# Kernel optimization log

Measured on AMD Instinct MI355X. Metric: run time of the kernel, lower is better.

## Reference

```python
import jax, jax.numpy as jnp
import numpy as np

B, L, D = 2, 2048, 2048
H, HKV, HD = 32, 8, 64
EPS = 1e-5
THETA = 1000000.0


def rms_norm(x, w):
    # normalize over last dim (head_dim)
    return x * jax.lax.rsqrt(jnp.mean(x * x, axis=-1, keepdims=True) + EPS) * w


def apply_rope(t):
    # t: (B, heads, L, HD); non-traditional (half-split) RoPE, offset=0
    half = HD // 2
    inv_freq = THETA ** (-jnp.arange(0, HD, 2, dtype=jnp.float32) / HD)  # (half,)
    ang = jnp.arange(L, dtype=jnp.float32)[:, None] * inv_freq           # (L, half)
    cos, sin = jnp.cos(ang), jnp.sin(ang)
    x1, x2 = t[..., :half], t[..., half:]
    return jnp.concatenate([x1 * cos - x2 * sin, x2 * cos + x1 * sin], axis=-1)


def setup_inputs() -> dict:
    key = jax.random.key(0)
    ks = jax.random.split(key, 5)
    s = 0.02
    return {
        "x": jax.random.normal(ks[0], (B, L, D), dtype=jnp.float32),
        "Wq": jax.random.normal(ks[1], (D, H * HD), dtype=jnp.float32) * s,
        "Wk": jax.random.normal(ks[2], (D, HKV * HD), dtype=jnp.float32) * s,
        "Wv": jax.random.normal(ks[3], (D, HKV * HD), dtype=jnp.float32) * s,
        "Wo": jax.random.normal(ks[4], (H * HD, D), dtype=jnp.float32) * s,
        "q_norm_w": jnp.ones((HD,), dtype=jnp.float32),
        "k_norm_w": jnp.ones((HD,), dtype=jnp.float32),
    }


def reference(x, Wq, Wk, Wv, Wo, q_norm_w, k_norm_w):
    scale = HD ** -0.5
    g = H // HKV  # GQA group size
    # projections
    q = (x @ Wq).reshape(B, L, H, HD)
    k = (x @ Wk).reshape(B, L, HKV, HD)
    v = (x @ Wv).reshape(B, L, HKV, HD)
    # per-head RMSNorm, then to (B, heads, L, HD)
    q = jnp.transpose(rms_norm(q, q_norm_w), (0, 2, 1, 3))
    k = jnp.transpose(rms_norm(k, k_norm_w), (0, 2, 1, 3))
    v = jnp.transpose(v, (0, 2, 1, 3))
    # RoPE
    q = apply_rope(q)
    k = apply_rope(k)
    # grouped-query attention with causal mask
    qg = q.reshape(B, HKV, g, L, HD)
    scores = jnp.einsum('bhgqd,bhkd->bhgqk', qg, k) * scale  # (B,HKV,g,L,L)
    causal = jnp.tril(jnp.ones((L, L), dtype=bool))
    scores = jnp.where(causal, scores, jnp.finfo(scores.dtype).min)
    probs = jax.nn.softmax(scores, axis=-1)
    out = jnp.einsum('bhgqk,bhkd->bhgqd', probs, v)           # (B,HKV,g,L,HD)
    out = jnp.transpose(out.reshape(B, H, L, HD), (0, 2, 1, 3)).reshape(B, L, H * HD)
    return out @ Wo
```

## Files before the change

kernel.cpp:

```cpp
#include <hip/hip_runtime.h>
#include <math.h>
#include <stdint.h>

#define B_ 2
#define L_ 2048
#define D_ 2048
#define H_ 32
#define HKV_ 8
#define HD_ 64
#define EPS_ 1e-5f

typedef _Float16 half_t;
typedef __attribute__((ext_vector_type(8))) _Float16 half8_t;
typedef __attribute__((ext_vector_type(4))) _Float16 half4_t;
typedef __attribute__((ext_vector_type(4))) float float4_t;

typedef const __attribute__((address_space(1))) uint32_t glb_u32;
typedef __attribute__((address_space(3))) uint32_t lds_u32;
#define GLOAD_LDS16(gp, lp) \
  __builtin_amdgcn_global_load_lds((glb_u32*)(gp), (lds_u32*)(lp), 16, 0, 0)

__device__ __forceinline__ float4_t fmax4(float4_t a, float4_t b) {
  float4_t r;
  r[0] = fmaxf(a[0], b[0]); r[1] = fmaxf(a[1], b[1]);
  r[2] = fmaxf(a[2], b[2]); r[3] = fmaxf(a[3], b[3]);
  return r;
}

__global__ __launch_bounds__(256) void prep_all(
    const float* __restrict__ x,
    const float* __restrict__ Wq, const float* __restrict__ Wk,
    const float* __restrict__ Wv, const float* __restrict__ Wo,
    half_t* __restrict__ xh,
    half_t* __restrict__ Wqt, half_t* __restrict__ Wkt,
    half_t* __restrict__ Wvt, half_t* __restrict__ Wot)
{
  __shared__ float tile[64][65];
  const int t = threadIdx.x;
  int id = blockIdx.x;

  if (id < 4096) {
    size_t i = ((size_t)id * 256 + t) * 8;
    float4 v0 = *(const float4*)&x[i];
    float4 v1 = *(const float4*)&x[i + 4];
    half8_t h;
    h[0] = (half_t)v0.x; h[1] = (half_t)v0.y; h[2] = (half_t)v0.z; h[3] = (half_t)v0.w;
    h[4] = (half_t)v1.x; h[5] = (half_t)v1.y; h[6] = (half_t)v1.z; h[7] = (half_t)v1.w;
    *(half8_t*)&xh[i] = h;
    return;
  }
  id -= 4096;
  const float* W; half_t* Wt; int N;
  if (id < 1024)      { W = Wq; Wt = Wqt; N = 2048; }
  else if (id < 1280) { id -= 1024; W = Wk; Wt = Wkt; N = 512; }
  else if (id < 1536) { id -= 1280; W = Wv; Wt = Wvt; N = 512; }
  else                { id -= 1536; W = Wo; Wt = Wot; N = 2048; }
  const int K = 2048;
  int tk = id & 31, tn = id >> 5;
  int k0 = tk * 64, n0 = tn * 64;

  int rr = t >> 6, cc = t & 63;
#pragma unroll
  for (int i = 0; i < 16; i++)
    tile[rr + i * 4][cc] = W[(size_t)(k0 + rr + i * 4) * N + n0 + cc];
  __syncthreads();

  int rn = t >> 2, q4 = (t & 3) * 16;
  half8_t h0, h1;
#pragma unroll
  for (int u = 0; u < 8; u++) h0[u] = (half_t)tile[q4 + u][rn];
#pragma unroll
  for (int u = 0; u < 8; u++) h1[u] = (half_t)tile[q4 + 8 + u][rn];
  *(half8_t*)&Wt[(size_t)(n0 + rn) * K + k0 + q4]     = h0;
  *(half8_t*)&Wt[(size_t)(n0 + rn) * K + k0 + q4 + 8] = h1;
}

template <typename CT>
__device__ __forceinline__ void gemm_tile_f16(
    const half_t* __restrict__ A, const half_t* __restrict__ Bt,
    CT* __restrict__ C, int K, int ldc, int row0, int col0)
{
  __shared__ __align__(16) half_t As[128 * 32];
  __shared__ __align__(16) half_t Bs[128 * 32];
  const int t    = threadIdx.x;
  const int lane = t & 63;
  const int w    = t >> 6;
  const int quad = lane >> 4, c = lane & 15;
  const int wm = (w >> 1) * 64, wn = (w & 1) * 64;

  float4_t acc[4][4];
#pragma unroll
  for (int i = 0; i < 4; i++)
#pragma unroll
    for (int j = 0; j < 4; j++) acc[i][j] = (float4_t){0.f, 0.f, 0.f, 0.f};

  const int srow = w * 32 + (lane >> 2);
  const int scol = (lane & 3) * 8;
  const half_t* Ag0 = A  + (size_t)(row0 + srow) * K + scol;
  const half_t* Ag1 = Ag0 + (size_t)16 * K;
  const half_t* Bg0 = Bt + (size_t)(col0 + srow) * K + scol;
  const half_t* Bg1 = Bg0 + (size_t)16 * K;
  half_t* As_w0 = &As[(w * 32) * 32];
  half_t* As_w1 = &As[(w * 32 + 16) * 32];
  half_t* Bs_w0 = &Bs[(w * 32) * 32];
  half_t* Bs_w1 = &Bs[(w * 32 + 16) * 32];

  for (int k0 = 0; k0 < K; k0 += 32) {
    __syncthreads();
    GLOAD_LDS16(Ag0 + k0, As_w0);
    GLOAD_LDS16(Ag1 + k0, As_w1);
    GLOAD_LDS16(Bg0 + k0, Bs_w0);
    GLOAD_LDS16(Bg1 + k0, Bs_w1);
    __syncthreads();

    half8_t af[4], bf[4];
#pragma unroll
    for (int i = 0; i < 4; i++)
      af[i] = *(const half8_t*)&As[(wm + i * 16 + c) * 32 + quad * 8];
#pragma unroll
    for (int j = 0; j < 4; j++)
      bf[j] = *(const half8_t*)&Bs[(wn + j * 16 + c) * 32 + quad * 8];
#pragma unroll
    for (int i = 0; i < 4; i++)
#pragma unroll
      for (int j = 0; j < 4; j++)
        acc[i][j] = __builtin_amdgcn_mfma_f32_16x16x32_f16(af[i], bf[j], acc[i][j], 0, 0, 0);
  }

#pragma unroll
  for (int i = 0; i < 4; i++)
#pragma unroll
    for (int r = 0; r < 4; r++) {
      CT* Cp = C + (size_t)(row0 + wm + i * 16 + quad * 4 + r) * ldc + col0 + wn + c;
#pragma unroll
      for (int j = 0; j < 4; j++)
        Cp[j * 16] = (CT)acc[i][j][r];
    }
}

__global__ __launch_bounds__(256) void qkv_gemm_h(
    const half_t* __restrict__ xh,
    const half_t* __restrict__ Wqt, const half_t* __restrict__ Wkt,
    const half_t* __restrict__ Wvt,
    half_t* __restrict__ qh, half_t* __restrict__ kh, half_t* __restrict__ vh)
{
  int bx = blockIdx.x;
  const half_t* Bt; half_t* C; int ldc, col0;
  if (bx < 16)      { Bt = Wqt; C = qh; ldc = H_ * HD_;   col0 = bx * 128; }
  else if (bx < 20) { Bt = Wkt; C = kh; ldc = HKV_ * HD_; col0 = (bx - 16) * 128; }
  else              { Bt = Wvt; C = vh; ldc = HKV_ * HD_; col0 = (bx - 20) * 128; }
  gemm_tile_f16<half_t>(xh, Bt, C, D_, ldc, blockIdx.y * 128, col0);
}

__global__ __launch_bounds__(256) void out_gemm_h(
    const half_t* __restrict__ attn, const half_t* __restrict__ Wot,
    float* __restrict__ out)
{
  gemm_tile_f16<float>(attn, Wot, out, H_ * HD_, D_, blockIdx.y * 128, blockIdx.x * 128);
}

__device__ __forceinline__ void norm_rope_body(
    half_t* buf, const float* w, int wave, int nheads, int lognh,
    int lane, float oscale)
{
  int head  = wave & (nheads - 1);
  int token = wave >> lognh;
  int l     = token & (L_ - 1);

  size_t idx = (size_t)token * (nheads * HD_) + head * HD_ + lane;
  float x = (float)buf[idx];

  float ss = x * x;
#pragma unroll
  for (int off = 32; off; off >>= 1) ss += __shfl_xor(ss, off);
  float xn = x * rsqrtf(ss * (1.0f / HD_) + EPS_) * w[lane];

  float partner = __shfl_xor(xn, 32);
  int   fi = lane & 31;
  float inv_freq = exp2f((float)fi * -0.622862853f);
  float ang = (float)l * inv_freq;
  float cv = cosf(ang), sv = sinf(ang);
  float res = (lane < 32) ? (xn * cv - partner * sv) : (xn * cv + partner * sv);
  buf[idx] = (half_t)(res * oscale);
}

__global__ __launch_bounds__(256) void postproc(
    half_t* __restrict__ qh, half_t* __restrict__ kh,
    const half_t* __restrict__ vh, half_t* __restrict__ vt,
    const float* __restrict__ qw, const float* __restrict__ kw)
{
  const int t = threadIdx.x;
  int id = blockIdx.x;
  if (id < 32768) {
    int wave = id * 4 + (t >> 6);
    norm_rope_body(qh, qw, wave, H_, 5, t & 63, 0.180336880f);
    return;
  }
  id -= 32768;
  if (id < 8192) {
    int wave = id * 4 + (t >> 6);
    norm_rope_body(kh, kw, wave, HKV_, 3, t & 63, 1.0f);
    return;
  }
  id -= 8192;
  int kk0 = (id & 31) * 64, kvh = (id >> 5) & 7, b = id >> 8;
  int d = t >> 2, uu = t & 3;
  const half_t* src = vh + (size_t)(b * L_) * (HKV_ * HD_) + kvh * HD_ + d;
  half_t* dst = vt + ((size_t)((b * HKV_ + kvh) * HD_ + d)) * L_ + kk0 + uu * 16;
  half_t vals[16];
#pragma unroll
  for (int u = 0; u < 16; u++)
    vals[u] = src[(size_t)(kk0 + uu * 16 + u) * (HKV_ * HD_)];
#pragma unroll
  for (int u = 0; u < 16; u += 4)
    *(half4_t*)&dst[u] = *(half4_t*)&vals[u];
}

__global__ __launch_bounds__(512) void flash_mfma2(
    const half_t* __restrict__ Qh, const half_t* __restrict__ Kh,
    const half_t* __restrict__ Vt, half_t* __restrict__ Oa)
{
  __shared__ __align__(16) half_t Ks[64][72];
  __shared__ __align__(16) half_t Vs[64][72];
  __shared__ __align__(16) half_t Ps[128][72];
  __shared__ __align__(16) float  Ab[128];

  const int t    = threadIdx.x;
  const int w    = t >> 6;
  const int lane = t & 63;
  const int quad = lane >> 4;
  const int c    = lane & 15;
  const int h = blockIdx.y, b = blockIdx.z;
  const int kvh = h >> 2;

  const half_t* kbase = Kh + (size_t)(b * L_) * (HKV_ * HD_) + kvh * HD_;
  const half_t* vbase = Vt + (size_t)((b * HKV_ + kvh) * HD_) * L_;
  const int sr = t >> 3;
  const int su = (t & 7) * 8;

  for (int pass = 0; pass < 2; pass++) {
    const int qb  = pass ? (15 - (int)blockIdx.x) : (int)blockIdx.x;
    const int q0  = qb * 128;
    const int wq0 = q0 + w * 16;

    half8_t qf0, qf1;
    {
      const half_t* qp = Qh + ((size_t)(b * L_ + wq0 + c)) * (H_ * HD_) + h * HD_;
      qf0 = *(const half8_t*)&qp[quad * 8];
      qf1 = *(const half8_t*)&qp[32 + quad * 8];
    }

    float4_t o[4];
#pragma unroll
    for (int dt = 0; dt < 4; dt++) o[dt] = (float4_t){0.f, 0.f, 0.f, 0.f};
    float mm = -__builtin_inff();
    float ll = 0.f;

    half8_t kr, vr;
    kr = *(const half8_t*)(kbase + (size_t)sr * (HKV_ * HD_) + su);
    vr = *(const half8_t*)(vbase + (size_t)sr * L_ + su);

    const int last = (q0 + 127) >> 6;
    for (int kt = 0; kt <= last; kt++) {
      const int kk0 = kt * 64;
      __syncthreads();
      *(half8_t*)&Ks[sr][su] = kr;
      *(half8_t*)&Vs[sr][su] = vr;
      __syncthreads();
      if (kt < last) {
        kr = *(const half8_t*)(kbase + (size_t)(kk0 + 64 + sr) * (HKV_ * HD_) + su);
        vr = *(const half8_t*)(vbase + (size_t)sr * L_ + kk0 + 64 + su);
      }
      if (kk0 > wq0 + 15) continue;

      float4_t S[4];
#pragma unroll
      for (int tt = 0; tt < 4; tt++) {
        half8_t kf0 = *(const half8_t*)&Ks[tt * 16 + c][quad * 8];
        half8_t kf1 = *(const half8_t*)&Ks[tt * 16 + c][32 + quad * 8];
        float4_t s = (float4_t){0.f, 0.f, 0.f, 0.f};
        s = __builtin_amdgcn_mfma_f32_16x16x32_f16(kf0, qf0, s, 0, 0, 0);
        s = __builtin_amdgcn_mfma_f32_16x16x32_f16(kf1, qf1, s, 0, 0, 0);
        S[tt] = s;
      }

      if (kk0 + 63 > wq0) {
#pragma unroll
        for (int tt = 0; tt < 4; tt++) {
          int base = kk0 + tt * 16 + quad * 4 - (wq0 + c);
#pragma unroll
          for (int r = 0; r < 4; r++)
            if (base + r > 0) S[tt][r] = -__builtin_inff();
        }
      }

      {
        float4_t m4 = fmax4(fmax4(S[0], S[1]), fmax4(S[2], S[3]));
        float mloc = fmaxf(fmaxf(m4[0], m4[1]), fmaxf(m4[2], m4[3]));
        mloc = fmaxf(mloc, __shfl_xor(mloc, 16));
        mloc = fmaxf(mloc, __shfl_xor(mloc, 32));
        float mnew = fmaxf(mm, mloc);
        float al = exp2f(mm - mnew);
        mm = mnew;
#pragma unroll
        for (int tt = 0; tt < 4; tt++) {
#pragma unroll
          for (int r = 0; r < 4; r++) S[tt][r] = exp2f(S[tt][r] - mnew);
          half4_t pv;
#pragma unroll
          for (int r = 0; r < 4; r++) pv[r] = (half_t)S[tt][r];
          *(half4_t*)&Ps[w * 16 + c][tt * 16 + quad * 4] = pv;
        }
        float4_t s4 = S[0] + S[1] + S[2] + S[3];
        float ls = (s4[0] + s4[1]) + (s4[2] + s4[3]);
        ls += __shfl_xor(ls, 16);
        ls += __shfl_xor(ls, 32);
        ll = ll * al + ls;
        if (quad == 0) Ab[w * 16 + c] = al;
      }

      {
        float4_t av = *(const float4_t*)&Ab[w * 16 + quad * 4];
#pragma unroll
        for (int dt = 0; dt < 4; dt++)
#pragma unroll
          for (int r = 0; r < 4; r++) o[dt][r] *= av[r];
      }

      half8_t pf0 = *(const half8_t*)&Ps[w * 16 + c][quad * 8];
      half8_t pf1 = *(const half8_t*)&Ps[w * 16 + c][32 + quad * 8];
#pragma unroll
      for (int dt = 0; dt < 4; dt++) {
        half8_t vf0 = *(const half8_t*)&Vs[dt * 16 + c][quad * 8];
        half8_t vf1 = *(const half8_t*)&Vs[dt * 16 + c][32 + quad * 8];
        o[dt] = __builtin_amdgcn_mfma_f32_16x16x32_f16(pf0, vf0, o[dt], 0, 0, 0);
        o[dt] = __builtin_amdgcn_mfma_f32_16x16x32_f16(pf1, vf1, o[dt], 0, 0, 0);
      }
    }

    if (quad == 0) Ab[w * 16 + c] = ll;
    {
      float4_t lv = *(const float4_t*)&Ab[w * 16 + quad * 4];
#pragma unroll
      for (int r = 0; r < 4; r++) {
        float inv = 1.0f / lv[r];
        half_t* op = Oa + ((size_t)(b * L_ + wq0 + quad * 4 + r)) * (H_ * HD_)
                   + h * HD_ + c;
#pragma unroll
        for (int dt = 0; dt < 4; dt++)
          op[dt * 16] = (half_t)(o[dt][r] * inv);
      }
    }
  }
}

extern "C" void kernel_launch(void* const* d_in, const int* in_sizes, int n_in,
                              void* d_out, int out_size, void* d_ws, size_t ws_size,
                              hipStream_t stream)
{
  const float* x  = (const float*)d_in[0];
  const float* Wq = (const float*)d_in[1];
  const float* Wk = (const float*)d_in[2];
  const float* Wv = (const float*)d_in[3];
  const float* Wo = (const float*)d_in[4];
  const float* qw = (const float*)d_in[5];
  const float* kw = (const float*)d_in[6];
  float* out = (float*)d_out;

  const size_t XN = (size_t)B_ * L_ * D_;
  const size_t QN = (size_t)B_ * L_ * H_ * HD_;
  const size_t KN = (size_t)B_ * L_ * HKV_ * HD_;
  const size_t WQ = (size_t)D_ * H_ * HD_;
  const size_t WK = (size_t)D_ * HKV_ * HD_;

  half_t* p   = (half_t*)d_ws;
  half_t* xh  = p;  p += XN;
  half_t* Wqt = p;  p += WQ;
  half_t* Wkt = p;  p += WK;
  half_t* Wvt = p;  p += WK;
  half_t* Wot = p;  p += WQ;
  half_t* qh  = p;  p += QN;
  half_t* kh  = p;  p += KN;
  half_t* vh  = p;  p += KN;
  half_t* vt  = p;  p += KN;
  half_t* attn = xh;

  prep_all<<<6656, 256, 0, stream>>>(x, Wq, Wk, Wv, Wo, xh, Wqt, Wkt, Wvt, Wot);

  qkv_gemm_h<<<dim3(24, 32), 256, 0, stream>>>(xh, Wqt, Wkt, Wvt, qh, kh, vh);

  postproc<<<32768 + 8192 + 512, 256, 0, stream>>>(qh, kh, vh, vt, qw, kw);

  flash_mfma2<<<dim3(8, H_, B_), 512, 0, stream>>>(qh, kh, vt, attn);

  out_gemm_h<<<dim3(16, 32), 256, 0, stream>>>(attn, Wot, out);
}
```

Baseline: 349.4 us.

## Lazy softmax rescale, MFMA row-sum, packed f16 convert, and MFMA priority hints

The attention kernel now rescales the output accumulator only when some row max grows by more than 8 (log2 units), which skips most of the exp and multiply work for the running max. The row-sum of probabilities is computed by an extra MFMA against a vector of ones instead of shuffle reductions. P is converted with packed round-toward-zero f16 conversion, and s_setprio is raised around the MFMA blocks. The lazy threshold lets unnormalised probabilities reach up to 2^8 in f16, a small precision risk, and the added MFMA costs extra matrix-core work.

After: 335.5 us. 1.04x faster.

```diff
diff --git a/kernel.cpp b/kernel.cpp
--- a/kernel.cpp
+++ b/kernel.cpp
@@ -25,6 +25,11 @@
   r[0] = fmaxf(a[0], b[0]); r[1] = fmaxf(a[1], b[1]);
   r[2] = fmaxf(a[2], b[2]); r[3] = fmaxf(a[3], b[3]);
   return r;
+}
+
+__device__ __forceinline__ uint32_t pk_f16(float a, float b) {
+  auto p = __builtin_amdgcn_cvt_pkrtz(a, b);
+  return __builtin_bit_cast(uint32_t, p);
 }
 
 __global__ __launch_bounds__(256) void prep_all(
@@ -238,6 +243,10 @@
   const int sr = t >> 3;
   const int su = (t & 7) * 8;
 
+  half8_t ones;
+#pragma unroll
+  for (int u = 0; u < 8; u++) ones[u] = (half_t)1.0f;
+
   for (int pass = 0; pass < 2; pass++) {
     const int qb  = pass ? (15 - (int)blockIdx.x) : (int)blockIdx.x;
     const int q0  = qb * 128;
@@ -250,11 +259,10 @@
       qf1 = *(const half8_t*)&qp[32 + quad * 8];
     }
 
-    float4_t o[4];
-#pragma unroll
-    for (int dt = 0; dt < 4; dt++) o[dt] = (float4_t){0.f, 0.f, 0.f, 0.f};
+    float4_t o[5];
+#pragma unroll
+    for (int dt = 0; dt < 5; dt++) o[dt] = (float4_t){0.f, 0.f, 0.f, 0.f};
     float mm = -__builtin_inff();
-    float ll = 0.f;
 
     half8_t kr, vr;
     kr = *(const half8_t*)(kbase + (size_t)sr * (HKV_ * HD_) + su);
@@ -274,6 +282,7 @@
       if (kk0 > wq0 + 15) continue;
 
       float4_t S[4];
+      __builtin_amdgcn_s_setprio(1);
 #pragma unroll
       for (int tt = 0; tt < 4; tt++) {
         half8_t kf0 = *(const half8_t*)&Ks[tt * 16 + c][quad * 8];
@@ -283,6 +292,7 @@
         s = __builtin_amdgcn_mfma_f32_16x16x32_f16(kf1, qf1, s, 0, 0, 0);
         S[tt] = s;
       }
+      __builtin_amdgcn_s_setprio(0);
 
       if (kk0 + 63 > wq0) {
 #pragma unroll
@@ -299,36 +309,33 @@
         float mloc = fmaxf(fmaxf(m4[0], m4[1]), fmaxf(m4[2], m4[3]));
         mloc = fmaxf(mloc, __shfl_xor(mloc, 16));
         mloc = fmaxf(mloc, __shfl_xor(mloc, 32));
-        float mnew = fmaxf(mm, mloc);
-        float al = exp2f(mm - mnew);
-        mm = mnew;
+        if (__any(mloc > mm + 8.0f)) {
+          float mnew = fmaxf(mm, mloc);
+          float al = exp2f(mm - mnew);
+          mm = mnew;
+          if (quad == 0) Ab[w * 16 + c] = al;
+          float4_t av = *(const float4_t*)&Ab[w * 16 + quad * 4];
+#pragma unroll
+          for (int dt = 0; dt < 5; dt++)
+#pragma unroll
+            for (int r = 0; r < 4; r++) o[dt][r] *= av[r];
+        }
 #pragma unroll
         for (int tt = 0; tt < 4; tt++) {
 #pragma unroll
-          for (int r = 0; r < 4; r++) S[tt][r] = exp2f(S[tt][r] - mnew);
-          half4_t pv;
-#pragma unroll
-          for (int r = 0; r < 4; r++) pv[r] = (half_t)S[tt][r];
-          *(half4_t*)&Ps[w * 16 + c][tt * 16 + quad * 4] = pv;
+          for (int r = 0; r < 4; r++) S[tt][r] = exp2f(S[tt][r] - mm);
+          uint2 pw;
+          pw.x = pk_f16(S[tt][0], S[tt][1]);
+          pw.y = pk_f16(S[tt][2], S[tt][3]);
+          *(uint2*)&Ps[w * 16 + c][tt * 16 + quad * 4] = pw;
         }
-        float4_t s4 = S[0] + S[1] + S[2] + S[3];
-        float ls = (s4[0] + s4[1]) + (s4[2] + s4[3]);
-        ls += __shfl_xor(ls, 16);
-        ls += __shfl_xor(ls, 32);
-        ll = ll * al + ls;
-        if (quad == 0) Ab[w * 16 + c] = al;
-      }
-
-      {
-        float4_t av = *(const float4_t*)&Ab[w * 16 + quad * 4];
-#pragma unroll
-        for (int dt = 0; dt < 4; dt++)
-#pragma unroll
-          for (int r = 0; r < 4; r++) o[dt][r] *= av[r];
       }
 
       half8_t pf0 = *(const half8_t*)&Ps[w * 16 + c][quad * 8];
       half8_t pf1 = *(const half8_t*)&Ps[w * 16 + c][32 + quad * 8];
+      __builtin_amdgcn_s_setprio(1);
+      o[4] = __builtin_amdgcn_mfma_f32_16x16x32_f16(pf0, ones, o[4], 0, 0, 0);
+      o[4] = __builtin_amdgcn_mfma_f32_16x16x32_f16(pf1, ones, o[4], 0, 0, 0);
 #pragma unroll
       for (int dt = 0; dt < 4; dt++) {
         half8_t vf0 = *(const half8_t*)&Vs[dt * 16 + c][quad * 8];
@@ -336,20 +343,17 @@
         o[dt] = __builtin_amdgcn_mfma_f32_16x16x32_f16(pf0, vf0, o[dt], 0, 0, 0);
         o[dt] = __builtin_amdgcn_mfma_f32_16x16x32_f16(pf1, vf1, o[dt], 0, 0, 0);
       }
+      __builtin_amdgcn_s_setprio(0);
     }
 
-    if (quad == 0) Ab[w * 16 + c] = ll;
-    {
-      float4_t lv = *(const float4_t*)&Ab[w * 16 + quad * 4];
-#pragma unroll
-      for (int r = 0; r < 4; r++) {
-        float inv = 1.0f / lv[r];
-        half_t* op = Oa + ((size_t)(b * L_ + wq0 + quad * 4 + r)) * (H_ * HD_)
-                   + h * HD_ + c;
-#pragma unroll
-        for (int dt = 0; dt < 4; dt++)
-          op[dt * 16] = (half_t)(o[dt][r] * inv);
-      }
+#pragma unroll
+    for (int r = 0; r < 4; r++) {
+      float inv = 1.0f / o[4][r];
+      half_t* op = Oa + ((size_t)(b * L_ + wq0 + quad * 4 + r)) * (H_ * HD_)
+                 + h * HD_ + c;
+#pragma unroll
+      for (int dt = 0; dt < 4; dt++)
+        op[dt * 16] = (half_t)(o[dt][r] * inv);
     }
   }
 }
```
